# Kernel tuning notes

Measured on AMD Instinct MI355X. Metric: run time of the kernel, lower is better.

Reference implementation:

```python
import jax, jax.numpy as jnp
import numpy as np

T, B, M = 512, 64, 512
DM = 384  # memory_size
DX = 384  # input_size
H = 192   # hidden_size
A = 192   # attention_size


def setup_inputs() -> dict:
    key = jax.random.key(0)
    ks = iter(jax.random.split(key, 24))

    def rn(shape, s):
        return jax.random.normal(next(ks), shape, jnp.float32) * s

    inp = {
        "memory": rn((M, B, DM), 1.0),
        "memory_mask": jnp.ones((M, B), jnp.bool_),
        "input": rn((T, B, DX), 1.0),
    }
    for suf in ("fw", "bw"):
        inp[f"Wm_{suf}"] = rn((DM, A), 0.08)
        inp[f"Wx_{suf}"] = rn((DX, A), 0.08)
        inp[f"Wh_{suf}"] = rn((H, A), 0.08)
        inp[f"v_{suf}"] = rn((A,), 0.08)
        inp[f"Wg_{suf}"] = rn((DX + DM, DX + DM), 0.05)
        inp[f"Wih_{suf}"] = rn((DX + DM, 3 * H), 0.05)
        inp[f"Whh_{suf}"] = rn((H, 3 * H), 0.08)
        inp[f"bih_{suf}"] = jnp.zeros((3 * H,), jnp.float32)
        inp[f"bhh_{suf}"] = jnp.zeros((3 * H,), jnp.float32)
    return inp


def _direction(x, memory, mask, Wm, Wx, Wh, v, Wg, Wih, Whh, bih, bhh):
    """Unroll one gated-attention GRU direction. x:[T,B,DX], memory:[M,B,DM]."""
    mem_proj = jnp.einsum('mbd,da->mba', memory, Wm)  # [M,B,A], hoisted out of scan
    x_proj = jnp.einsum('tbd,da->tba', x, Wx)         # [T,B,A]
    h0 = jnp.zeros((x.shape[1], Whh.shape[0]), x.dtype)
    neg = jnp.asarray(-1e9, x.dtype)

    def step(h, xs):
        x_t, xp_t = xs
        # additive attention over memory positions
        s = jnp.einsum('mba,a->mb', jnp.tanh(mem_proj + xp_t[None] + (h @ Wh)[None]), v)
        s = jnp.where(mask, s, neg)
        a = jax.nn.softmax(s, axis=0)                 # softmax over M
        c = jnp.einsum('mb,mbd->bd', a, memory)       # context [B,DM]
        xc = jnp.concatenate([x_t, c], axis=-1)       # [B,DX+DM]
        xc = jax.nn.sigmoid(xc @ Wg) * xc             # R-net input gate
        gi = xc @ Wih + bih
        gh = h @ Whh + bhh
        ir, iz, inn = jnp.split(gi, 3, axis=-1)
        hr, hz, hn = jnp.split(gh, 3, axis=-1)
        r = jax.nn.sigmoid(ir + hr)
        z = jax.nn.sigmoid(iz + hz)
        n = jnp.tanh(inn + r * hn)
        h_new = (1 - z) * n + z * h                   # torch GRUCell update
        return h_new, h_new

    _, ys = jax.lax.scan(step, h0, (x, x_proj))
    return ys  # [T,B,H]


def reference(memory, memory_mask, input,
              Wm_fw, Wx_fw, Wh_fw, v_fw, Wg_fw, Wih_fw, Whh_fw, bih_fw, bhh_fw,
              Wm_bw, Wx_bw, Wh_bw, v_bw, Wg_bw, Wih_bw, Whh_bw, bih_bw, bhh_bw):
    out_fw = _direction(input, memory, memory_mask,
                        Wm_fw, Wx_fw, Wh_fw, v_fw, Wg_fw, Wih_fw, Whh_fw, bih_fw, bhh_fw)
    out_bw = _direction(input[::-1], memory, memory_mask,
                        Wm_bw, Wx_bw, Wh_bw, v_bw, Wg_bw, Wih_bw, Whh_bw, bih_bw, bhh_bw)[::-1]
    # dropout is identity in eval mode
    return jnp.concatenate([out_fw, out_bw], axis=-1)  # [T,B,2H]
```

## Files before the change

### kernel.cpp

```cpp
#include <hip/hip_runtime.h>
#include <hip/hip_fp16.h>

#define TT 512
#define MM 512
#define NWG 256

__device__ __forceinline__ float fast_sigmoid(float x) {
  float e = __expf(-x);
  return __builtin_amdgcn_rcpf(1.f + e);
}
__device__ __forceinline__ float fast_tanh(float x) {
  float e = __expf(2.f * x);
  return 1.f - 2.f * __builtin_amdgcn_rcpf(e + 1.f);
}
__device__ __forceinline__ float2 h2f2(unsigned u) {
  __half2 h = *reinterpret_cast<__half2*>(&u);
  return __half22float2(h);
}
__device__ __forceinline__ unsigned pack2(float x, float y) {
  __half2 h = __floats2half2_rn(x, y);
  return *reinterpret_cast<unsigned*>(&h);
}

typedef _Float16 hf2_t __attribute__((ext_vector_type(2)));
__device__ __forceinline__ float fdot2f(unsigned a, unsigned b, float c) {
#if __has_builtin(__builtin_amdgcn_fdot2)
  union U { unsigned u; hf2_t h; };
  U ua, ub; ua.u = a; ub.u = b;
  return __builtin_amdgcn_fdot2(ua.h, ub.h, c, false);
#else
  float2 fa = h2f2(a), fb = h2f2(b);
  return fmaf(fa.x, fb.x, fmaf(fa.y, fb.y, c));
#endif
}

template<int K, int S>
__device__ __forceinline__ float dotpipe(const unsigned* __restrict__ w,
                                         const unsigned* __restrict__ x2) {
  unsigned A[12], B[12];
  float acc[4] = {0.f, 0.f, 0.f, 0.f};
  #pragma unroll
  for (int i = 0; i < 12; ++i) A[i] = w[(size_t)i * S];
  #pragma unroll 1
  for (int k = 0; k < K; k += 24) {
    #pragma unroll
    for (int i = 0; i < 12; ++i) B[i] = w[(size_t)(k + 12 + i) * S];
    #pragma unroll
    for (int i = 0; i < 12; ++i) acc[i & 3] = fdot2f(A[i], x2[k + i], acc[i & 3]);
    if (k + 24 < K) {
      #pragma unroll
      for (int i = 0; i < 12; ++i) A[i] = w[(size_t)(k + 24 + i) * S];
    }
    #pragma unroll
    for (int i = 0; i < 12; ++i) acc[i & 3] = fdot2f(B[i], x2[k + 12 + i], acc[i & 3]);
  }
  return (acc[0] + acc[1]) + (acc[2] + acc[3]);
}

__device__ __forceinline__ void ast(float* p, float v) {
  __hip_atomic_store(p, v, __ATOMIC_RELAXED, __HIP_MEMORY_SCOPE_AGENT);
}
__device__ __forceinline__ float ald(const float* p) {
  return __hip_atomic_load(p, __ATOMIC_RELAXED, __HIP_MEMORY_SCOPE_AGENT);
}
__device__ __forceinline__ void astu(unsigned* p, unsigned v) {
  __hip_atomic_store(p, v, __ATOMIC_RELAXED, __HIP_MEMORY_SCOPE_AGENT);
}
__device__ __forceinline__ unsigned aldu(const unsigned* p) {
  return __hip_atomic_load(p, __ATOMIC_RELAXED, __HIP_MEMORY_SCOPE_AGENT);
}
__device__ __forceinline__ void astull(unsigned long long* p, unsigned long long v) {
  __hip_atomic_store(p, v, __ATOMIC_RELAXED, __HIP_MEMORY_SCOPE_AGENT);
}
__device__ __forceinline__ unsigned long long aldull(const unsigned long long* p) {
  return __hip_atomic_load(p, __ATOMIC_RELAXED, __HIP_MEMORY_SCOPE_AGENT);
}
union F2U { unsigned long long u; float f[2]; };

struct ProjParams {
  const float* X[4]; const float* W[4]; __half* C[4]; int rev[4]; int transp[4];
};

__global__ __launch_bounds__(192) void proj_kernel(ProjParams pp) {
  __shared__ float xs[32 * 384];
  const int job = blockIdx.y;
  const float* __restrict__ X = pp.X[job];
  const float* __restrict__ W = pp.W[job];
  __half* __restrict__ C = pp.C[job];
  const int rev = pp.rev[job];
  const int transp = pp.transp[job];
  const int r0 = blockIdx.x * 32;
  const int tid = threadIdx.x;

  for (int idx = tid; idx < 32 * 384; idx += 192) {
    int r = idx / 384, k = idx - r * 384;
    int row = r0 + r;
    int srow = row;
    if (rev) { int t = row >> 6, b2 = row & 63; srow = ((TT - 1 - t) << 6) | b2; }
    xs[idx] = X[(size_t)srow * 384 + k];
  }
  __syncthreads();

  float acc[32];
  #pragma unroll
  for (int r = 0; r < 32; ++r) acc[r] = 0.f;
  for (int k = 0; k < 384; ++k) {
    float w = W[k * 192 + tid];
    #pragma unroll
    for (int r = 0; r < 32; ++r) acc[r] = fmaf(xs[r * 384 + k], w, acc[r]);
  }
  #pragma unroll
  for (int r = 0; r < 32; ++r) {
    int row = r0 + r;
    size_t di = transp ? (((size_t)(row & 63) * MM + (row >> 6)) * 192 + tid)
                       : ((size_t)row * 192 + tid);
    C[di] = __float2half(acc[r]);
  }
}

__global__ __launch_bounds__(384) void memcvt_kernel(const float* __restrict__ src,
                                                     __half* __restrict__ dst) {
  int m = blockIdx.x, b = blockIdx.y, d = threadIdx.x;
  dst[((size_t)b * MM + m) * 384 + d] = __float2half(src[((size_t)m * 64 + b) * 384 + d]);
}

struct WcvtParams { const float* src[8]; unsigned* dst[8]; int tot[8]; int N[8]; };
__global__ __launch_bounds__(256) void wcvt_kernel(WcvtParams wp) {
  int job = blockIdx.y;
  const float* __restrict__ s = wp.src[job];
  unsigned* __restrict__ d = wp.dst[job];
  int n = wp.N[job], tot = wp.tot[job];
  for (int i = blockIdx.x * 256 + threadIdx.x; i < tot; i += gridDim.x * 256) {
    int k2 = i / n, j = i - k2 * n;
    d[i] = pack2(s[(size_t)(2 * k2) * n + j], s[(size_t)(2 * k2 + 1) * n + j]);
  }
}

#define L_MP     0
#define L_REDP   98304
#define L_SH384  110592
#define L_Q      112128
#define L_XCF    112896
#define L_XC2    115968
#define L_G2     117504
#define L_GIS    119040
#define L_GHS    120192
#define L_HF     121344
#define L_H2     122112
#define L_VS     122496
#define L_BIH    123264
#define L_BHH    124416
#define L_ZP     125568
#define L_MISC   125600
#define L_ES     125632
#define SCAN_LDS 126656
static_assert(SCAN_LDS <= 160 * 1024, "LDS overflow");

struct ScanParams {
  const float* input;
  const unsigned* memt;
  const unsigned* mpt[2];
  const __half* xp[2];
  const unsigned* Wh2[2];
  const unsigned* Wg2[2];
  const unsigned* Wih2[2];
  const unsigned* Whh2[2];
  const float* v[2];
  const float* bih[2];
  const float* bhh[2];
  unsigned long long* ectx;
  float* ez;
  unsigned* gmail;
  unsigned* hmail;
  unsigned* flags;
  float* out;
};

__global__ __launch_bounds__(512, 1) void scan_kernel(ScanParams p) {
  extern __shared__ char smem[];
  __half*   mp_s   = (__half*)(smem + L_MP);
  float*    redp   = (float*)(smem + L_REDP);
  float*    sh384  = (float*)(smem + L_SH384);
  float*    q_s    = (float*)(smem + L_Q);
  float*    xc_f   = (float*)(smem + L_XCF);
  unsigned* xc2_s  = (unsigned*)(smem + L_XC2);
  unsigned* g2_s   = (unsigned*)(smem + L_G2);
  float*    gis    = (float*)(smem + L_GIS);
  float*    ghs    = (float*)(smem + L_GHS);
  float*    h_f    = (float*)(smem + L_HF);
  unsigned* h2_s   = (unsigned*)(smem + L_H2);
  float*    v_s    = (float*)(smem + L_VS);
  float*    bih_s  = (float*)(smem + L_BIH);
  float*    bhh_s  = (float*)(smem + L_BHH);
  float*    zp_s   = (float*)(smem + L_ZP);
  float*    e_s    = (float*)(smem + L_ES);

  const int g = blockIdx.x;
  const int xcd = g & 7;
  const int slot = g >> 3;
  const int dir = xcd >> 2;
  const int idx = (xcd & 3) * 32 + slot;
  const int b = idx & 63;
  const int half = idx >> 6;
  const int tid = threadIdx.x;
  const int lane = tid & 63;
  const int wv = tid >> 6;

  const unsigned* __restrict__ Wh2  = p.Wh2[dir];
  const unsigned* __restrict__ Wg2  = p.Wg2[dir];
  const unsigned* __restrict__ Wih2 = p.Wih2[dir];
  const unsigned* __restrict__ Whh2 = p.Whh2[dir];
  const __half* __restrict__ xp = p.xp[dir];
  const int m0 = half * 256;

  const int idx_my = (dir * 2 + half) * 64 + b;
  const int idx_p  = (dir * 2 + (half ^ 1)) * 64 + b;
  unsigned long long* myctx_u = p.ectx + (size_t)idx_my * 2 * 192;
  const unsigned long long* pctx_u = p.ectx + (size_t)idx_p * 2 * 192;
  float* myz0 = p.ez + (size_t)idx_my * 2;
  const float* pz0 = p.ez + (size_t)idx_p * 2;
  unsigned* gmail_my = p.gmail + (size_t)idx_my * 2 * 192;
  const unsigned* gmail_p = p.gmail + (size_t)idx_p * 2 * 192;
  unsigned* hmail_my = p.hmail + (size_t)idx_my * 2 * 48;
  const unsigned* hmail_p = p.hmail + (size_t)idx_p * 2 * 48;
  unsigned* fctx_my = p.flags + idx_my;        const unsigned* fctx_p = p.flags + idx_p;
  unsigned* fg_my   = p.flags + 256 + idx_my;  const unsigned* fg_p   = p.flags + 256 + idx_p;
  unsigned* fh_my   = p.flags + 512 + idx_my;  const unsigned* fh_p   = p.flags + 512 + idx_p;

  {
    const unsigned* mpu = p.mpt[dir] + ((size_t)b * MM + m0) * 96;
    unsigned* mpd = (unsigned*)mp_s;
    for (int i = tid; i < 256 * 96; i += 512) mpd[i] = mpu[i];
    if (tid < 192) { h_f[tid] = 0.f; v_s[tid] = p.v[dir][tid]; }
    if (tid < 96) h2_s[tid] = 0u;
    if (tid < 288) {
      int c3 = tid / 96, jj = tid - c3 * 96;
      int col = c3 * 192 + 96 * half + jj;
      bih_s[tid] = p.bih[dir][col];
      bhh_s[tid] = p.bhh[dir][col];
    }
  }
  __syncthreads();
  const float v0 = v_s[lane], v1 = v_s[lane + 64], v2 = v_s[lane + 128];

  #pragma unroll 1
  for (int t = 0; t < TT; ++t) {
    const int par = t & 1;
    if (tid < 384) {
      const int kh = (tid >= 192);
      const int a = tid - 192 * kh;
      sh384[tid] = dotpipe<48, 192>(Wh2 + (size_t)kh * 48 * 192 + a, h2_s + kh * 48);
    }
    __syncthreads();
    if (tid < 192)
      q_s[tid] = __half2float(xp[((size_t)t * 64 + b) * 192 + tid]) + sh384[tid] + sh384[192 + tid];
    __syncthreads();

    {
      const float q0 = q_s[lane], q1 = q_s[lane + 64], q2 = q_s[lane + 128];
      float zacc = 0.f;
      const __half* mph = mp_s + (wv * 32) * 192;
      #pragma unroll 4
      for (int i = 0; i < 32; ++i) {
        const __half* r = mph + i * 192;
        float s = v0 * fast_tanh(__half2float(r[lane]) + q0)
                + v1 * fast_tanh(__half2float(r[lane + 64]) + q1)
                + v2 * fast_tanh(__half2float(r[lane + 128]) + q2);
        #pragma unroll
        for (int off = 32; off > 0; off >>= 1) s += __shfl_xor(s, off, 64);
        float e = __expf(s);
        zacc += e;
        if (lane == 0) e_s[wv * 32 + i] = e;
      }
      if (lane == 0) zp_s[wv] = zacc;
    }
    __syncthreads();
    {
      float ca[8] = {0, 0, 0, 0, 0, 0, 0, 0};
      if (lane < 48) {
        const uint4* mrow4 = (const uint4*)(p.memt + ((size_t)b * MM + m0 + wv * 32) * 192) + lane;
        const float* es = e_s + wv * 32;
        #pragma unroll 8
        for (int i = 0; i < 32; ++i) {
          uint4 mv = mrow4[(size_t)i * 48];
          float e = es[i];
          float2 f0 = h2f2(mv.x), f1 = h2f2(mv.y), f2 = h2f2(mv.z), f3 = h2f2(mv.w);
          ca[0] = fmaf(e, f0.x, ca[0]); ca[1] = fmaf(e, f0.y, ca[1]);
          ca[2] = fmaf(e, f1.x, ca[2]); ca[3] = fmaf(e, f1.y, ca[3]);
          ca[4] = fmaf(e, f2.x, ca[4]); ca[5] = fmaf(e, f2.y, ca[5]);
          ca[6] = fmaf(e, f3.x, ca[6]); ca[7] = fmaf(e, f3.y, ca[7]);
        }
        float2* rp2 = (float2*)(redp + wv * 384 + 8 * lane);
        rp2[0] = make_float2(ca[0], ca[1]);
        rp2[1] = make_float2(ca[2], ca[3]);
        rp2[2] = make_float2(ca[4], ca[5]);
        rp2[3] = make_float2(ca[6], ca[7]);
      }
    }
    __syncthreads();

    const int xt = dir ? (TT - 1 - t) : t;
    const float* xrow = p.input + ((size_t)xt * 64 + b) * 384;
    if (tid < 192) {
      float cm0 = 0.f, cm1 = 0.f;
      const float2* rp2 = (const float2*)redp;
      #pragma unroll
      for (int k = 0; k < 8; ++k) {
        float2 v2r = rp2[k * 192 + tid];
        cm0 += v2r.x; cm1 += v2r.y;
      }
      sh384[2 * tid] = cm0; sh384[2 * tid + 1] = cm1;
      F2U u; u.f[0] = cm0; u.f[1] = cm1;
      astull(myctx_u + par * 192 + tid, u.u);
      float2 xi = ((const float2*)xrow)[tid];
      xc_f[2 * tid] = xi.x; xc_f[2 * tid + 1] = xi.y;
      xc2_s[tid] = pack2(xi.x, xi.y);
    }
    if (tid == 0) {
      float zs = 0.f;
      #pragma unroll
      for (int k = 0; k < 8; ++k) zs += zp_s[k];
      ast(myz0 + par, zs);
    }
    __syncthreads();
    if (tid == 0) astu(fctx_my, (unsigned)(t + 1));

    float eacc = 0.f;
    if (tid < 384) {
      const int col = 384 * half + tid;
      eacc = dotpipe<192, 768>(Wg2 + col, xc2_s);
    } else {
      for (int jj = tid - 384; jj < 288; jj += 128) {
        const int c3 = jj / 96;
        const int col = c3 * 192 + 96 * half + (jj - c3 * 96);
        ghs[jj] = dotpipe<96, 576>(Whh2 + col, h2_s) + bhh_s[jj];
      }
    }
    if (tid < 192) {
      while (aldu(fctx_p) < (unsigned)(t + 1)) __builtin_amdgcn_s_sleep(1);
      F2U u; u.u = aldull(pctx_u + par * 192 + tid);
      float zl = ((zp_s[0] + zp_s[1]) + (zp_s[2] + zp_s[3]))
               + ((zp_s[4] + zp_s[5]) + (zp_s[6] + zp_s[7]));
      float pz = ald(pz0 + par);
      float iz = __builtin_amdgcn_rcpf(zl + pz);
      float x0 = (sh384[2 * tid] + u.f[0]) * iz;
      float x1 = (sh384[2 * tid + 1] + u.f[1]) * iz;
      xc_f[384 + 2 * tid] = x0;
      xc_f[384 + 2 * tid + 1] = x1;
      xc2_s[192 + tid] = pack2(x0, x1);
    }
    __syncthreads();

    if (tid < 384) {
      const int col = 384 * half + tid;
      eacc += dotpipe<192, 768>(Wg2 + (size_t)192 * 768 + col, xc2_s + 192);
      sh384[tid] = fast_sigmoid(eacc) * xc_f[col];
    }
    __syncthreads();

    if (tid < 192) {
      unsigned pk = pack2(sh384[2 * tid], sh384[2 * tid + 1]);
      g2_s[192 * half + tid] = pk;
      astu(gmail_my + par * 192 + tid, pk);
    }
    __syncthreads();
    if (tid == 0) astu(fg_my, (unsigned)(t + 1));

    float gacc = 0.f;
    if (tid < 288) {
      const int c3 = tid / 96, jj = tid - c3 * 96;
      const int col = c3 * 192 + 96 * half + jj;
      gacc = dotpipe<192, 576>(Wih2 + (size_t)(192 * half) * 576 + col, g2_s + 192 * half);
    }
    if (tid < 192) {
      while (aldu(fg_p) < (unsigned)(t + 1)) __builtin_amdgcn_s_sleep(1);
      g2_s[192 * (1 - half) + tid] = aldu(gmail_p + par * 192 + tid);
    }
    __syncthreads();

    if (tid < 288) {
      const int c3 = tid / 96, jj = tid - c3 * 96;
      const int col = c3 * 192 + 96 * half + jj;
      gis[tid] = gacc + bih_s[tid]
               + dotpipe<192, 576>(Wih2 + (size_t)(192 * (1 - half)) * 576 + col,
                                   g2_s + 192 * (1 - half));
    }
    __syncthreads();

    if (tid < 48) {
      const int j0 = 96 * half + 2 * tid;
      float r0 = fast_sigmoid(gis[2 * tid]       + ghs[2 * tid]);
      float z0 = fast_sigmoid(gis[96 + 2 * tid]  + ghs[96 + 2 * tid]);
      float n0 = fast_tanh(gis[192 + 2 * tid] + r0 * ghs[192 + 2 * tid]);
      float hn0 = (1.f - z0) * n0 + z0 * h_f[j0];
      float r1 = fast_sigmoid(gis[2 * tid + 1]      + ghs[2 * tid + 1]);
      float z1 = fast_sigmoid(gis[96 + 2 * tid + 1] + ghs[96 + 2 * tid + 1]);
      float n1 = fast_tanh(gis[192 + 2 * tid + 1] + r1 * ghs[192 + 2 * tid + 1]);
      float hn1 = (1.f - z1) * n1 + z1 * h_f[j0 + 1];
      h_f[j0] = hn0; h_f[j0 + 1] = hn1;
      int trow = dir ? (TT - 1 - t) : t;
      float2* orow = (float2*)(p.out + ((size_t)trow * 64 + b) * 384 + dir * 192);
      orow[48 * half + tid] = make_float2(hn0, hn1);
      unsigned pk = pack2(hn0, hn1);
      h2_s[48 * half + tid] = pk;
      astu(hmail_my + par * 48 + tid, pk);
    }
    __syncthreads();
    if (tid == 0) astu(fh_my, (unsigned)(t + 1));
    if (tid < 48) {
      while (aldu(fh_p) < (unsigned)(t + 1)) __builtin_amdgcn_s_sleep(1);
      h2_s[48 * (1 - half) + tid] = aldu(hmail_p + par * 48 + tid);
    }
    __syncthreads();
  }
}

extern "C" void kernel_launch(void* const* d_in, const int* in_sizes, int n_in,
                              void* d_out, int out_size, void* d_ws, size_t ws_size,
                              hipStream_t stream) {
  (void)in_sizes; (void)n_in; (void)out_size;
  const float* memory = (const float*)d_in[0];
  const float* input  = (const float*)d_in[2];
  const float* Wm[2]  = {(const float*)d_in[3],  (const float*)d_in[12]};
  const float* Wx[2]  = {(const float*)d_in[4],  (const float*)d_in[13]};
  const float* Wh[2]  = {(const float*)d_in[5],  (const float*)d_in[14]};
  const float* v[2]   = {(const float*)d_in[6],  (const float*)d_in[15]};
  const float* Wg[2]  = {(const float*)d_in[7],  (const float*)d_in[16]};
  const float* Wih[2] = {(const float*)d_in[8],  (const float*)d_in[17]};
  const float* Whh[2] = {(const float*)d_in[9],  (const float*)d_in[18]};
  const float* bih[2] = {(const float*)d_in[10], (const float*)d_in[19]};
  const float* bhh[2] = {(const float*)d_in[11], (const float*)d_in[20]};

  char* ws = (char*)d_ws;
  const size_t OFF_FLAGS = 0;
  const size_t OFF_EZ    = 4096;
  const size_t OFF_GMAIL = 6144;
  const size_t OFF_HMAIL = 792576;
  const size_t OFF_ECTX  = 989184;
  const size_t OFF_MPT0  = 1775616;
  const size_t OFF_MPT1  = OFF_MPT0 + 12582912;
  const size_t OFF_XP0   = OFF_MPT1 + 12582912;
  const size_t OFF_XP1   = OFF_XP0 + 12582912;
  const size_t OFF_MT    = OFF_XP1 + 12582912;
  const size_t OFF_WG0   = OFF_MT + 25165824;
  const size_t OFF_WG1   = OFF_WG0 + 1179648;
  const size_t OFF_WIH0  = OFF_WG1 + 1179648;
  const size_t OFF_WIH1  = OFF_WIH0 + 884736;
  const size_t OFF_WHH0  = OFF_WIH1 + 884736;
  const size_t OFF_WHH1  = OFF_WHH0 + 221184;
  const size_t OFF_WH0   = OFF_WHH1 + 221184;
  const size_t OFF_WH1   = OFF_WH0 + 73728;
  const size_t NEEDED    = OFF_WH1 + 73728;
  if (ws_size < NEEDED) return;

  unsigned* flags = (unsigned*)(ws + OFF_FLAGS);
  float* ez    = (float*)(ws + OFF_EZ);
  unsigned* gmail = (unsigned*)(ws + OFF_GMAIL);
  unsigned* hmail = (unsigned*)(ws + OFF_HMAIL);
  unsigned long long* ectx = (unsigned long long*)(ws + OFF_ECTX);
  __half* mpt0 = (__half*)(ws + OFF_MPT0);
  __half* mpt1 = (__half*)(ws + OFF_MPT1);
  __half* xp0  = (__half*)(ws + OFF_XP0);
  __half* xp1  = (__half*)(ws + OFF_XP1);
  __half* memt = (__half*)(ws + OFF_MT);
  unsigned* wg2[2]  = {(unsigned*)(ws + OFF_WG0),  (unsigned*)(ws + OFF_WG1)};
  unsigned* wih2[2] = {(unsigned*)(ws + OFF_WIH0), (unsigned*)(ws + OFF_WIH1)};
  unsigned* whh2[2] = {(unsigned*)(ws + OFF_WHH0), (unsigned*)(ws + OFF_WHH1)};
  unsigned* wh2[2]  = {(unsigned*)(ws + OFF_WH0),  (unsigned*)(ws + OFF_WH1)};

  hipFuncSetAttribute(reinterpret_cast<const void*>(scan_kernel),
                      hipFuncAttributeMaxDynamicSharedMemorySize, SCAN_LDS);

  hipMemsetAsync(ws + OFF_FLAGS, 0, 4096, stream);

  ProjParams pp;
  pp.X[0] = memory; pp.W[0] = Wm[0]; pp.C[0] = mpt0; pp.rev[0] = 0; pp.transp[0] = 1;
  pp.X[1] = memory; pp.W[1] = Wm[1]; pp.C[1] = mpt1; pp.rev[1] = 0; pp.transp[1] = 1;
  pp.X[2] = input;  pp.W[2] = Wx[0]; pp.C[2] = xp0;  pp.rev[2] = 0; pp.transp[2] = 0;
  pp.X[3] = input;  pp.W[3] = Wx[1]; pp.C[3] = xp1;  pp.rev[3] = 1; pp.transp[3] = 0;
  proj_kernel<<<dim3(1024, 4), dim3(192), 0, stream>>>(pp);
  memcvt_kernel<<<dim3(MM, 64), dim3(384), 0, stream>>>(memory, memt);

  WcvtParams wp;
  for (int d = 0; d < 2; ++d) {
    wp.src[d]     = Wg[d];  wp.dst[d]     = wg2[d];  wp.tot[d]     = 384 * 768; wp.N[d]     = 768;
    wp.src[2 + d] = Wih[d]; wp.dst[2 + d] = wih2[d]; wp.tot[2 + d] = 384 * 576; wp.N[2 + d] = 576;
    wp.src[4 + d] = Whh[d]; wp.dst[4 + d] = whh2[d]; wp.tot[4 + d] = 96 * 576;  wp.N[4 + d] = 576;
    wp.src[6 + d] = Wh[d];  wp.dst[6 + d] = wh2[d];  wp.tot[6 + d] = 96 * 192;  wp.N[6 + d] = 192;
  }
  wcvt_kernel<<<dim3(288, 8), dim3(256), 0, stream>>>(wp);

  ScanParams sp;
  sp.input = input;
  sp.memt = (const unsigned*)memt;
  sp.mpt[0] = (const unsigned*)mpt0; sp.mpt[1] = (const unsigned*)mpt1;
  sp.xp[0] = xp0; sp.xp[1] = xp1;
  for (int d = 0; d < 2; ++d) {
    sp.Wh2[d] = wh2[d]; sp.Wg2[d] = wg2[d]; sp.Wih2[d] = wih2[d]; sp.Whh2[d] = whh2[d];
    sp.v[d] = v[d]; sp.bih[d] = bih[d]; sp.bhh[d] = bhh[d];
  }
  sp.ectx = ectx; sp.ez = ez; sp.gmail = gmail; sp.hmail = hmail; sp.flags = flags;
  sp.out = (float*)d_out;
  scan_kernel<<<dim3(NWG), dim3(512), SCAN_LDS, stream>>>(sp);
}
```

Before: 22.29 ms.

## Split each batch-direction scan across four workgroups instead of two

Raises the persistent scan grid from 256 to 512 workgroups. Each (direction, batch) recurrence now runs on four workgroups, each holding a quarter of the memory positions and a quarter of the gate/hidden columns. Context partials, gate outputs and hidden-state slices are exchanged through global mailboxes with flag spinning among the four peers. LDS per workgroup is halved so two can share a CU, which cuts per-step attention and matvec work per workgroup. In exchange there are more cross-workgroup synchronisations and global round-trips per timestep, and the extra barrier latency could outweigh the smaller per-workgroup work.

```diff
diff --git a/kernel.cpp b/kernel.cpp
--- a/kernel.cpp
+++ b/kernel.cpp
@@ -3,7 +3,7 @@
 
 #define TT 512
 #define MM 512
-#define NWG 256
+#define NWG 512
 
 __device__ __forceinline__ float fast_sigmoid(float x) {
   float e = __expf(-x);
@@ -137,24 +137,22 @@
 }
 
 #define L_MP     0
-#define L_REDP   98304
-#define L_SH384  110592
-#define L_Q      112128
-#define L_XCF    112896
-#define L_XC2    115968
-#define L_G2     117504
-#define L_GIS    119040
-#define L_GHS    120192
-#define L_HF     121344
-#define L_H2     122112
-#define L_VS     122496
-#define L_BIH    123264
-#define L_BHH    124416
-#define L_ZP     125568
-#define L_MISC   125600
-#define L_ES     125632
-#define SCAN_LDS 126656
-static_assert(SCAN_LDS <= 160 * 1024, "LDS overflow");
+#define L_REDP   49152
+#define L_SH384  61440
+#define L_Q      62976
+#define L_XCF    63744
+#define L_XC2    66816
+#define L_G2     68352
+#define L_GHS    69888
+#define L_HF     70528
+#define L_H2     70784
+#define L_VS     71168
+#define L_BIH    71936
+#define L_BHH    72576
+#define L_ZP     73216
+#define L_ES     73248
+#define SCAN_LDS 73760
+static_assert(SCAN_LDS <= 80 * 1024, "need <=80KB for 2 WGs/CU");
 
 struct ScanParams {
   const float* input;
@@ -176,7 +174,7 @@
   float* out;
 };
 
-__global__ __launch_bounds__(512, 1) void scan_kernel(ScanParams p) {
+__global__ __launch_bounds__(512, 4) void scan_kernel(ScanParams p) {
   extern __shared__ char smem[];
   __half*   mp_s   = (__half*)(smem + L_MP);
   float*    redp   = (float*)(smem + L_REDP);
@@ -185,7 +183,6 @@
   float*    xc_f   = (float*)(smem + L_XCF);
   unsigned* xc2_s  = (unsigned*)(smem + L_XC2);
   unsigned* g2_s   = (unsigned*)(smem + L_G2);
-  float*    gis    = (float*)(smem + L_GIS);
   float*    ghs    = (float*)(smem + L_GHS);
   float*    h_f    = (float*)(smem + L_HF);
   unsigned* h2_s   = (unsigned*)(smem + L_H2);
@@ -199,9 +196,8 @@
   const int xcd = g & 7;
   const int slot = g >> 3;
   const int dir = xcd >> 2;
-  const int idx = (xcd & 3) * 32 + slot;
-  const int b = idx & 63;
-  const int half = idx >> 6;
+  const int b = (xcd & 3) * 16 + (slot >> 2);
+  const int q = slot & 3;
   const int tid = threadIdx.x;
   const int lane = tid & 63;
   const int wv = tid >> 6;
@@ -211,31 +207,29 @@
   const unsigned* __restrict__ Wih2 = p.Wih2[dir];
   const unsigned* __restrict__ Whh2 = p.Whh2[dir];
   const __half* __restrict__ xp = p.xp[dir];
-  const int m0 = half * 256;
-
-  const int idx_my = (dir * 2 + half) * 64 + b;
-  const int idx_p  = (dir * 2 + (half ^ 1)) * 64 + b;
-  unsigned long long* myctx_u = p.ectx + (size_t)idx_my * 2 * 192;
-  const unsigned long long* pctx_u = p.ectx + (size_t)idx_p * 2 * 192;
-  float* myz0 = p.ez + (size_t)idx_my * 2;
-  const float* pz0 = p.ez + (size_t)idx_p * 2;
-  unsigned* gmail_my = p.gmail + (size_t)idx_my * 2 * 192;
-  const unsigned* gmail_p = p.gmail + (size_t)idx_p * 2 * 192;
-  unsigned* hmail_my = p.hmail + (size_t)idx_my * 2 * 48;
-  const unsigned* hmail_p = p.hmail + (size_t)idx_p * 2 * 48;
-  unsigned* fctx_my = p.flags + idx_my;        const unsigned* fctx_p = p.flags + idx_p;
-  unsigned* fg_my   = p.flags + 256 + idx_my;  const unsigned* fg_p   = p.flags + 256 + idx_p;
-  unsigned* fh_my   = p.flags + 512 + idx_my;  const unsigned* fh_p   = p.flags + 512 + idx_p;
+  const int m0 = 128 * q;
+
+  const int dqb = (dir * 64 + b) * 4;
+  const int dq_my = dqb + q;
+  const int dq1 = dqb + (q ^ 1), dq2 = dqb + (q ^ 2), dq3 = dqb + (q ^ 3);
+  unsigned long long* myctx = p.ectx + (size_t)dq_my * 2 * 192;
+  float* myz = p.ez + (size_t)dq_my * 2;
+  unsigned* mygm = p.gmail + (size_t)dq_my * 2 * 96;
+  unsigned* myhm = p.hmail + (size_t)dq_my * 2 * 24;
+  unsigned* fctx = p.flags;
+  unsigned* fg   = p.flags + 512;
+  unsigned* fh   = p.flags + 1024;
 
   {
     const unsigned* mpu = p.mpt[dir] + ((size_t)b * MM + m0) * 96;
     unsigned* mpd = (unsigned*)mp_s;
-    for (int i = tid; i < 256 * 96; i += 512) mpd[i] = mpu[i];
-    if (tid < 192) { h_f[tid] = 0.f; v_s[tid] = p.v[dir][tid]; }
+    for (int i = tid; i < 128 * 96; i += 512) mpd[i] = mpu[i];
+    if (tid < 192) v_s[tid] = p.v[dir][tid];
     if (tid < 96) h2_s[tid] = 0u;
-    if (tid < 288) {
-      int c3 = tid / 96, jj = tid - c3 * 96;
-      int col = c3 * 192 + 96 * half + jj;
+    if (tid < 48) h_f[tid] = 0.f;
+    if (tid < 144) {
+      int c3 = tid / 48, jj = tid - c3 * 48;
+      int col = c3 * 192 + 48 * q + jj;
       bih_s[tid] = p.bih[dir][col];
       bhh_s[tid] = p.bhh[dir][col];
     }
@@ -246,6 +240,7 @@
   #pragma unroll 1
   for (int t = 0; t < TT; ++t) {
     const int par = t & 1;
+    const unsigned gen = (unsigned)(t + 1);
     if (tid < 384) {
       const int kh = (tid >= 192);
       const int a = tid - 192 * kh;
@@ -259,9 +254,9 @@
     {
       const float q0 = q_s[lane], q1 = q_s[lane + 64], q2 = q_s[lane + 128];
       float zacc = 0.f;
-      const __half* mph = mp_s + (wv * 32) * 192;
+      const __half* mph = mp_s + (wv * 16) * 192;
       #pragma unroll 4
-      for (int i = 0; i < 32; ++i) {
+      for (int i = 0; i < 16; ++i) {
         const __half* r = mph + i * 192;
         float s = v0 * fast_tanh(__half2float(r[lane]) + q0)
                 + v1 * fast_tanh(__half2float(r[lane + 64]) + q1)
@@ -270,18 +265,17 @@
         for (int off = 32; off > 0; off >>= 1) s += __shfl_xor(s, off, 64);
         float e = __expf(s);
         zacc += e;
-        if (lane == 0) e_s[wv * 32 + i] = e;
+        if (lane == 0) e_s[wv * 16 + i] = e;
       }
       if (lane == 0) zp_s[wv] = zacc;
     }
-    __syncthreads();
     {
       float ca[8] = {0, 0, 0, 0, 0, 0, 0, 0};
       if (lane < 48) {
-        const uint4* mrow4 = (const uint4*)(p.memt + ((size_t)b * MM + m0 + wv * 32) * 192) + lane;
-        const float* es = e_s + wv * 32;
+        const uint4* mrow4 = (const uint4*)(p.memt + ((size_t)b * MM + m0 + wv * 16) * 192) + lane;
+        const float* es = e_s + wv * 16;
         #pragma unroll 8
-        for (int i = 0; i < 32; ++i) {
+        for (int i = 0; i < 16; ++i) {
           uint4 mv = mrow4[(size_t)i * 48];
           float e = es[i];
           float2 f0 = h2f2(mv.x), f1 = h2f2(mv.y), f2 = h2f2(mv.z), f3 = h2f2(mv.w);
@@ -311,40 +305,48 @@
       }
       sh384[2 * tid] = cm0; sh384[2 * tid + 1] = cm1;
       F2U u; u.f[0] = cm0; u.f[1] = cm1;
-      astull(myctx_u + par * 192 + tid, u.u);
+      astull(myctx + par * 192 + tid, u.u);
       float2 xi = ((const float2*)xrow)[tid];
       xc_f[2 * tid] = xi.x; xc_f[2 * tid + 1] = xi.y;
       xc2_s[tid] = pack2(xi.x, xi.y);
     }
     if (tid == 0) {
-      float zs = 0.f;
-      #pragma unroll
-      for (int k = 0; k < 8; ++k) zs += zp_s[k];
-      ast(myz0 + par, zs);
-    }
-    __syncthreads();
-    if (tid == 0) astu(fctx_my, (unsigned)(t + 1));
+      float zs = ((zp_s[0] + zp_s[1]) + (zp_s[2] + zp_s[3]))
+               + ((zp_s[4] + zp_s[5]) + (zp_s[6] + zp_s[7]));
+      ast(myz + par, zs);
+    }
+    __syncthreads();
+    if (tid == 0) astu(fctx + dq_my, gen);
 
     float eacc = 0.f;
     if (tid < 384) {
-      const int col = 384 * half + tid;
-      eacc = dotpipe<192, 768>(Wg2 + col, xc2_s);
-    } else {
-      for (int jj = tid - 384; jj < 288; jj += 128) {
-        const int c3 = jj / 96;
-        const int col = c3 * 192 + 96 * half + (jj - c3 * 96);
-        ghs[jj] = dotpipe<96, 576>(Whh2 + col, h2_s) + bhh_s[jj];
+      const int kq = tid / 192, col = tid - kq * 192;
+      const int gc = 192 * q + col;
+      eacc = dotpipe<96, 768>(Wg2 + (size_t)(kq * 96) * 768 + gc, xc2_s + kq * 96);
+    } else if (tid < 504) {
+      for (int jj = tid - 384; jj < 144; jj += 120) {
+        int c3 = jj / 48;
+        int colg = c3 * 192 + 48 * q + (jj - c3 * 48);
+        ghs[jj] = dotpipe<96, 576>(Whh2 + colg, h2_s) + bhh_s[jj];
       }
-    }
+    } else if (tid < 507) {
+      const int pdq = dqb + (q ^ (tid - 503));
+      while (aldu(fctx + pdq) < gen) __builtin_amdgcn_s_sleep(1);
+    }
+    __syncthreads();
+
     if (tid < 192) {
-      while (aldu(fctx_p) < (unsigned)(t + 1)) __builtin_amdgcn_s_sleep(1);
-      F2U u; u.u = aldull(pctx_u + par * 192 + tid);
+      F2U u1, u2, u3;
+      u1.u = aldull(p.ectx + ((size_t)dq1 * 2 + par) * 192 + tid);
+      u2.u = aldull(p.ectx + ((size_t)dq2 * 2 + par) * 192 + tid);
+      u3.u = aldull(p.ectx + ((size_t)dq3 * 2 + par) * 192 + tid);
       float zl = ((zp_s[0] + zp_s[1]) + (zp_s[2] + zp_s[3]))
                + ((zp_s[4] + zp_s[5]) + (zp_s[6] + zp_s[7]));
-      float pz = ald(pz0 + par);
+      float pz = ald(p.ez + (size_t)dq1 * 2 + par) + ald(p.ez + (size_t)dq2 * 2 + par)
+               + ald(p.ez + (size_t)dq3 * 2 + par);
       float iz = __builtin_amdgcn_rcpf(zl + pz);
-      float x0 = (sh384[2 * tid] + u.f[0]) * iz;
-      float x1 = (sh384[2 * tid + 1] + u.f[1]) * iz;
+      float x0 = (sh384[2 * tid] + (u1.f[0] + u2.f[0] + u3.f[0])) * iz;
+      float x1 = (sh384[2 * tid + 1] + (u1.f[1] + u2.f[1] + u3.f[1])) * iz;
       xc_f[384 + 2 * tid] = x0;
       xc_f[384 + 2 * tid + 1] = x1;
       xc2_s[192 + tid] = pack2(x0, x1);
@@ -352,64 +354,82 @@
     __syncthreads();
 
     if (tid < 384) {
-      const int col = 384 * half + tid;
-      eacc += dotpipe<192, 768>(Wg2 + (size_t)192 * 768 + col, xc2_s + 192);
-      sh384[tid] = fast_sigmoid(eacc) * xc_f[col];
-    }
-    __syncthreads();
-
-    if (tid < 192) {
-      unsigned pk = pack2(sh384[2 * tid], sh384[2 * tid + 1]);
-      g2_s[192 * half + tid] = pk;
-      astu(gmail_my + par * 192 + tid, pk);
-    }
-    __syncthreads();
-    if (tid == 0) astu(fg_my, (unsigned)(t + 1));
-
-    float gacc = 0.f;
+      const int kq = tid / 192, col = tid - kq * 192;
+      const int gc = 192 * q + col;
+      eacc += dotpipe<96, 768>(Wg2 + (size_t)(192 + kq * 96) * 768 + gc, xc2_s + 192 + kq * 96);
+      sh384[tid] = eacc;
+    }
+    __syncthreads();
+
+    if (tid < 96) {
+      int c0 = 2 * tid, c1 = 2 * tid + 1;
+      float g0 = fast_sigmoid(sh384[c0] + sh384[192 + c0]) * xc_f[192 * q + c0];
+      float g1 = fast_sigmoid(sh384[c1] + sh384[192 + c1]) * xc_f[192 * q + c1];
+      unsigned pk = pack2(g0, g1);
+      g2_s[96 * q + tid] = pk;
+      astu(mygm + par * 96 + tid, pk);
+    }
+    __syncthreads();
+    if (tid == 0) astu(fg + dq_my, gen);
+
+    if (tid < 144) {
+      int c3 = tid / 48;
+      int colg = c3 * 192 + 48 * q + (tid - c3 * 48);
+      redp[tid] = dotpipe<96, 576>(Wih2 + (size_t)(96 * q) * 576 + colg, g2_s + 96 * q);
+    } else if (tid >= 504 && tid < 507) {
+      const int pdq = dqb + (q ^ (tid - 503));
+      while (aldu(fg + pdq) < gen) __builtin_amdgcn_s_sleep(1);
+    }
+    __syncthreads();
+
     if (tid < 288) {
-      const int c3 = tid / 96, jj = tid - c3 * 96;
-      const int col = c3 * 192 + 96 * half + jj;
-      gacc = dotpipe<192, 576>(Wih2 + (size_t)(192 * half) * 576 + col, g2_s + 192 * half);
-    }
-    if (tid < 192) {
-      while (aldu(fg_p) < (unsigned)(t + 1)) __builtin_amdgcn_s_sleep(1);
-      g2_s[192 * (1 - half) + tid] = aldu(gmail_p + par * 192 + tid);
-    }
-    __syncthreads();
-
-    if (tid < 288) {
-      const int c3 = tid / 96, jj = tid - c3 * 96;
-      const int col = c3 * 192 + 96 * half + jj;
-      gis[tid] = gacc + bih_s[tid]
-               + dotpipe<192, 576>(Wih2 + (size_t)(192 * (1 - half)) * 576 + col,
-                                   g2_s + 192 * (1 - half));
-    }
-    __syncthreads();
-
-    if (tid < 48) {
-      const int j0 = 96 * half + 2 * tid;
-      float r0 = fast_sigmoid(gis[2 * tid]       + ghs[2 * tid]);
-      float z0 = fast_sigmoid(gis[96 + 2 * tid]  + ghs[96 + 2 * tid]);
-      float n0 = fast_tanh(gis[192 + 2 * tid] + r0 * ghs[192 + 2 * tid]);
-      float hn0 = (1.f - z0) * n0 + z0 * h_f[j0];
-      float r1 = fast_sigmoid(gis[2 * tid + 1]      + ghs[2 * tid + 1]);
-      float z1 = fast_sigmoid(gis[96 + 2 * tid + 1] + ghs[96 + 2 * tid + 1]);
-      float n1 = fast_tanh(gis[192 + 2 * tid + 1] + r1 * ghs[192 + 2 * tid + 1]);
-      float hn1 = (1.f - z1) * n1 + z1 * h_f[j0 + 1];
-      h_f[j0] = hn0; h_f[j0 + 1] = hn1;
+      int k = tid / 96, j = tid - k * 96;
+      int qq = q ^ (k + 1);
+      g2_s[96 * qq + j] = aldu(p.gmail + ((size_t)(dqb + qq) * 2 + par) * 96 + j);
+    }
+    __syncthreads();
+
+    if (tid < 432) {
+      int j3 = tid / 144, col = tid - j3 * 144;
+      int c3 = col / 48;
+      int colg = c3 * 192 + 48 * q + (col - c3 * 48);
+      int kqq = (q + 1 + j3) & 3;
+      redp[144 + tid] = dotpipe<96, 576>(Wih2 + (size_t)(96 * kqq) * 576 + colg, g2_s + 96 * kqq);
+    }
+    __syncthreads();
+
+    if (tid < 24) {
       int trow = dir ? (TT - 1 - t) : t;
-      float2* orow = (float2*)(p.out + ((size_t)trow * 64 + b) * 384 + dir * 192);
-      orow[48 * half + tid] = make_float2(hn0, hn1);
-      unsigned pk = pack2(hn0, hn1);
-      h2_s[48 * half + tid] = pk;
-      astu(hmail_my + par * 48 + tid, pk);
-    }
-    __syncthreads();
-    if (tid == 0) astu(fh_my, (unsigned)(t + 1));
-    if (tid < 48) {
-      while (aldu(fh_p) < (unsigned)(t + 1)) __builtin_amdgcn_s_sleep(1);
-      h2_s[48 * (1 - half) + tid] = aldu(hmail_p + par * 48 + tid);
+      float2* orow = (float2*)(p.out + ((size_t)trow * 64 + b) * 384 + dir * 192 + 48 * q);
+      float hn[2];
+      #pragma unroll
+      for (int s2 = 0; s2 < 2; ++s2) {
+        int jj = 2 * tid + s2;
+        float gi_r = redp[jj]       + redp[144 + 0 * 144 + jj] + redp[144 + 1 * 144 + jj] + redp[144 + 2 * 144 + jj] + bih_s[jj];
+        float gi_z = redp[48 + jj]  + redp[144 + 0 * 144 + 48 + jj] + redp[144 + 1 * 144 + 48 + jj] + redp[144 + 2 * 144 + 48 + jj] + bih_s[48 + jj];
+        float gi_n = redp[96 + jj]  + redp[144 + 0 * 144 + 96 + jj] + redp[144 + 1 * 144 + 96 + jj] + redp[144 + 2 * 144 + 96 + jj] + bih_s[96 + jj];
+        float r = fast_sigmoid(gi_r + ghs[jj]);
+        float z = fast_sigmoid(gi_z + ghs[48 + jj]);
+        float n = fast_tanh(gi_n + r * ghs[96 + jj]);
+        hn[s2] = (1.f - z) * n + z * h_f[jj];
+        h_f[jj] = hn[s2];
+      }
+      orow[tid] = make_float2(hn[0], hn[1]);
+      unsigned pk = pack2(hn[0], hn[1]);
+      h2_s[24 * q + tid] = pk;
+      astu(myhm + par * 24 + tid, pk);
+    }
+    __syncthreads();
+    if (tid == 0) astu(fh + dq_my, gen);
+    if (tid >= 504 && tid < 507) {
+      const int pdq = dqb + (q ^ (tid - 503));
+      while (aldu(fh + pdq) < gen) __builtin_amdgcn_s_sleep(1);
+    }
+    __syncthreads();
+    if (tid < 72) {
+      int k = tid / 24, j = tid - k * 24;
+      int qq = q ^ (k + 1);
+      h2_s[24 * qq + j] = aldu(p.hmail + ((size_t)(dqb + qq) * 2 + par) * 24 + j);
     }
     __syncthreads();
   }
@@ -433,11 +453,11 @@
 
   char* ws = (char*)d_ws;
   const size_t OFF_FLAGS = 0;
-  const size_t OFF_EZ    = 4096;
-  const size_t OFF_GMAIL = 6144;
-  const size_t OFF_HMAIL = 792576;
-  const size_t OFF_ECTX  = 989184;
-  const size_t OFF_MPT0  = 1775616;
+  const size_t OFF_EZ    = 8192;
+  const size_t OFF_GMAIL = 12288;
+  const size_t OFF_HMAIL = 405504;
+  const size_t OFF_ECTX  = 503808;
+  const size_t OFF_MPT0  = 2076672;
   const size_t OFF_MPT1  = OFF_MPT0 + 12582912;
   const size_t OFF_XP0   = OFF_MPT1 + 12582912;
   const size_t OFF_XP1   = OFF_XP0 + 12582912;
@@ -471,7 +491,7 @@
   hipFuncSetAttribute(reinterpret_cast<const void*>(scan_kernel),
                       hipFuncAttributeMaxDynamicSharedMemorySize, SCAN_LDS);
 
-  hipMemsetAsync(ws + OFF_FLAGS, 0, 4096, stream);
+  hipMemsetAsync(ws + OFF_FLAGS, 0, 8192, stream);
 
   ProjParams pp;
   pp.X[0] = memory; pp.W[0] = Wm[0]; pp.C[0] = mpt0; pp.rev[0] = 0; pp.transp[0] = 1;
```

Result: slower. 28.16 ms (+26.3%).
